# Kernel optimization log

Measured on AMD Instinct MI355X. Metric: run time of the kernel, lower is better.

The kernel has to match this reference:

```python
import jax, jax.numpy as jnp
import numpy as np

N = 131072          # events
N_OBS = 64          # observables
HID = [512, 512, 512]          # trunk hidden widths
SUB_HID = [512, 256]           # per-pair subnetwork hidden widths
P = 3                          # number of pairings


def _glorot(key, shape):
    fan_in, fan_out = shape[-2], shape[-1]
    lim = np.sqrt(6.0 / (fan_in + fan_out)).astype(np.float32)
    return jax.random.uniform(key, shape, jnp.float32, -lim, lim)


def setup_inputs() -> dict:
    key = jax.random.key(0)
    ks = jax.random.split(key, 16)
    x = jax.random.normal(ks[0], (N, N_OBS), jnp.float32)
    y = jax.random.randint(ks[1], (N,), 0, 3)
    pairs = jnp.array([[0, 1], [0, 2], [1, 2]], dtype=jnp.int32)
    # trunk params
    W0 = _glorot(ks[2], (N_OBS, HID[0])); b0 = jnp.zeros((HID[0],), jnp.float32)
    W1 = _glorot(ks[3], (HID[0], HID[1])); b1 = jnp.zeros((HID[1],), jnp.float32)
    W2 = _glorot(ks[4], (HID[1], HID[2])); b2 = jnp.zeros((HID[2],), jnp.float32)
    # stacked per-pair subnetwork params (all P subnets share shapes)
    SW0 = _glorot(ks[5], (P, HID[2], SUB_HID[0])); Sb0 = jnp.zeros((P, SUB_HID[0]), jnp.float32)
    SW1 = _glorot(ks[6], (P, SUB_HID[0], SUB_HID[1])); Sb1 = jnp.zeros((P, SUB_HID[1]), jnp.float32)
    SW2 = _glorot(ks[7], (P, SUB_HID[1], 1)); Sb2 = jnp.zeros((P, 1), jnp.float32)
    return {"x": x, "y": y, "pairs": pairs,
            "W0": W0, "b0": b0, "W1": W1, "b1": b1, "W2": W2, "b2": b2,
            "SW0": SW0, "Sb0": Sb0, "SW1": SW1, "Sb1": Sb1, "SW2": SW2, "Sb2": Sb2}


def reference(x, y, pairs, W0, b0, W1, b1, W2, b2, SW0, Sb0, SW1, Sb1, SW2, Sb2):
    relu = jax.nn.relu
    # Trunk. Note: in the torch module with dropout_prob>0, the first Linear sits at
    # layer index 1, so the activation is applied to the raw input as well (eval-mode
    # dropout == identity). We reproduce that exactly.
    h = relu(x) @ W0 + b0
    h = relu(h) @ W1 + b1
    repr_ = relu(h) @ W2 + b2                      # [N, HID[-1]]

    # Per-pair membership masks (jit-safe stand-in for the variable-size gather):
    # mask[p, n] = True iff y[n] is one of the two labels of pairing p.
    mask = (y[None, :] == pairs[:, 0:1]) | (y[None, :] == pairs[:, 1:2])  # [P, N] bool

    # Per-pair RatioModel subnetworks, batched over the pair dim.
    # Same activation-before-every-Linear pattern as the trunk (dropout indices).
    hs = jnp.einsum('nd,pdh->pnh', relu(repr_), SW0) + Sb0[:, None, :]
    hs = jnp.einsum('pnh,phk->pnk', relu(hs), SW1) + Sb1[:, None, :]
    logit = jnp.einsum('pnk,pko->pno', relu(hs), SW2) + Sb2[:, None, :]  # [P, N, 1]
    s_hat = jnp.clip(jax.nn.sigmoid(logit[..., 0]), 1e-9, None)          # [P, N]
    r_hat = (1.0 - s_hat) / s_hat                                        # [P, N]

    maskf = mask.astype(s_hat.dtype)
    return repr_, r_hat * maskf, s_hat * maskf, mask
```

## Files before the change

kernel.cpp:

```cpp
#include <hip/hip_runtime.h>
#include <stdint.h>

#define NE 131072

typedef __attribute__((ext_vector_type(8))) short bf16x8;
typedef __attribute__((ext_vector_type(4))) float f32x4;

static __device__ __forceinline__ unsigned short f2bf(float f) {
  unsigned u = __float_as_uint(f);
  u += 0x7FFF + ((u >> 16) & 1);
  return (unsigned short)(u >> 16);
}
static __device__ __forceinline__ float bf2f(unsigned short h) {
  return __uint_as_float((unsigned)h << 16);
}
static __device__ __forceinline__ void gload_lds16(const void* g, void* l) {
  __builtin_amdgcn_global_load_lds(
      (const __attribute__((address_space(1))) unsigned*)g,
      (__attribute__((address_space(3))) unsigned*)l, 16, 0, 0);
}

__global__ void weight_prep(const float* __restrict__ W0, const float* __restrict__ W1,
                            const float* __restrict__ W2, const float* __restrict__ SW0,
                            const float* __restrict__ SW1, const float* __restrict__ SW2,
                            unsigned short* W0t, unsigned short* W1t,
                            unsigned short* W2t, unsigned short* SW0t,
                            unsigned short* SW1t, unsigned short* SW2b) {
  __shared__ float tile[32][33];
  const int u = blockIdx.y;
  const float* src; unsigned short* dst; int K, Nc;
  if (u == 0)      { src = W0;  dst = W0t;  K = 64;  Nc = 512; }
  else if (u == 1) { src = W1;  dst = W1t;  K = 512; Nc = 512; }
  else if (u == 2) { src = W2;  dst = W2t;  K = 512; Nc = 512; }
  else if (u < 6)  { int p = u - 3; src = SW0 + (long)p * 512 * 512; dst = SW0t + (long)p * 512 * 512; K = 512; Nc = 512; }
  else if (u < 9)  { int p = u - 6; src = SW1 + (long)p * 512 * 256; dst = SW1t + (long)p * 256 * 512; K = 512; Nc = 256; }
  else             { int p = u - 9; src = SW2 + (long)p * 256;       dst = SW2b + (long)p * 256;       K = 256; Nc = 1; }
  const int tkn = K >> 5;
  const int tk = blockIdx.x % tkn, tn = blockIdx.x / tkn;
  if (tn >= ((Nc + 31) >> 5)) return;
  const int k0 = tk * 32, n0 = tn * 32;
  const int tx = threadIdx.x & 31, ty = threadIdx.x >> 5;
  if (n0 + tx < Nc)
#pragma unroll
    for (int j = 0; j < 4; ++j)
      tile[ty * 4 + j][tx] = src[(long)(k0 + ty * 4 + j) * Nc + n0 + tx];
  __syncthreads();
#pragma unroll
  for (int j = 0; j < 4; ++j) {
    int n = n0 + ty * 4 + j;
    if (n < Nc) dst[(long)n * K + k0 + tx] = f2bf(tile[tx][ty * 4 + j]);
  }
}

__global__ void relu_cvt_x(const float4* __restrict__ x,
                           ushort4* __restrict__ xb) {
  int i = blockIdx.x * blockDim.x + threadIdx.x;
  float4 v = x[i];
  ushort4 o;
  o.x = f2bf(fmaxf(v.x, 0.f));
  o.y = f2bf(fmaxf(v.y, 0.f));
  o.z = f2bf(fmaxf(v.z, 0.f));
  o.w = f2bf(fmaxf(v.w, 0.f));
  xb[i] = o;
}

__global__ void build_idx(const int* __restrict__ y, const int* __restrict__ pairs,
                          int chunkRows, int* __restrict__ idxL,
                          int* __restrict__ posA, int* __restrict__ cnts) {
  const int c = blockIdx.x, p = blockIdx.y;
  const int la = pairs[p * 2], lb = pairs[p * 2 + 1];
  const long r0 = (long)c * chunkRows;
  const long cb = r0;
  __shared__ int wbase[4];
  __shared__ int running;
  if (threadIdx.x == 0) running = 0;
  __syncthreads();
  const int lane = threadIdx.x & 63, wv = threadIdx.x >> 6;
  for (int it = 0; it < chunkRows / 256; ++it) {
    const int r = it * 256 + threadIdx.x;
    const int yv = y[r0 + r];
    const bool act = (yv == la) || (yv == lb);
    const unsigned long long m = __ballot(act);
    const int rank = __popcll(m & ((1ull << lane) - 1));
    if (lane == 0) wbase[wv] = __popcll(m);
    __syncthreads();
    int wb = 0;
#pragma unroll
    for (int w = 0; w < 4; ++w) wb += (w < wv) ? wbase[w] : 0;
    const int tot = wbase[0] + wbase[1] + wbase[2] + wbase[3];
    if (act) {
      const int posi = running + wb + rank;
      idxL[(long)p * NE + cb + posi] = r;
      posA[(long)p * NE + r0 + r] = (int)(cb + posi);
    } else {
      posA[(long)p * NE + r0 + r] = -1;
    }
    __syncthreads();
    if (threadIdx.x == 0) running += tot;
    __syncthreads();
  }
  const int cnt = running;
  if (threadIdx.x == 0) cnts[c * 3 + p] = cnt;
  const int padded = (cnt + 255) & ~255;
  const int last = (cnt > 0) ? idxL[(long)p * NE + cb + cnt - 1] : 0;
  for (int i = cnt + threadIdx.x; i < padded; i += 256)
    idxL[(long)p * NE + cb + i] = last;
}

__global__ __launch_bounds__(512, 4) void gemmT(
    const unsigned short* __restrict__ A, long aZ,
    const unsigned short* __restrict__ Bt, long bZ,
    const float* __restrict__ bias, long biasZ,
    float* __restrict__ outF,
    unsigned short* __restrict__ outA, long cZ,
    int K, int Nc,
    const unsigned short* __restrict__ w2, long w2Z,
    float* __restrict__ PB, long pbZ, int r0,
    const int* __restrict__ aIdx, long aIdxZ,
    const int* __restrict__ cnts) {
  __shared__ unsigned short lds[3 * 12288];
  __shared__ float part[4][128];
  const int z = blockIdx.z;
  const long brow = (long)blockIdx.x * 128;
  if (cnts) {
    const int cp = cnts[z];
    if ((int)brow >= ((cp + 255) & ~255)) return;
  }
  A += (long)z * aZ;
  Bt += (long)z * bZ;
  bias += (long)z * biasZ;
  if (outA) outA += (long)z * cZ;
  if (w2) { w2 += (long)z * w2Z; PB += (long)z * pbZ; }
  if (aIdx) aIdx += (long)z * aIdxZ;

  const int tid = threadIdx.x, wave = tid >> 6, lane = tid & 63;
  const int wm = wave >> 2, wn = wave & 3;
  const int lr = lane & 15, lh = lane >> 4;
  const int bcol = blockIdx.y * 256;
  const int nk = K >> 5;
  const int axr = (lh ^ ((lr >> 1) & 3)) * 8;

  const int arL = tid >> 2;
  const int arow = aIdx ? aIdx[brow + arL] : (int)(brow + arL);

  f32x4 acc[4][4];
#pragma unroll
  for (int m = 0; m < 4; ++m)
#pragma unroll
    for (int n = 0; n < 4; ++n) acc[m][n] = (f32x4){0.f, 0.f, 0.f, 0.f};

  auto STAGE = [&](int t) {
    if (t >= nk) return;
    unsigned short* dst = &lds[(t % 3) * 12288];
    const int k0 = t << 5;
    {
      const int c = tid;
      const int r = c >> 2;
      const int kc = (c & 3) ^ ((r >> 1) & 3);
      gload_lds16(A + (long)arow * K + k0 + kc * 8, &dst[(wave * 64) * 8]);
    }
#pragma unroll
    for (int i = 0; i < 2; ++i) {
      const int cb = i * 512 + wave * 64;
      const int c = cb + lane;
      const int r = c >> 2;
      const int kc = (c & 3) ^ ((r >> 1) & 3);
      gload_lds16(Bt + (long)(bcol + r) * K + k0 + kc * 8,
                  &dst[(512 + cb) * 8]);
    }
  };

  STAGE(0);
  STAGE(1);

  for (int t = 0; t < nk; ++t) {
    if (t < nk - 1)
      asm volatile("s_waitcnt vmcnt(3)" ::: "memory");
    else
      asm volatile("s_waitcnt vmcnt(0)" ::: "memory");
    __builtin_amdgcn_s_barrier();
    __builtin_amdgcn_sched_barrier(0);
    const unsigned short* buf = &lds[(t % 3) * 12288];
    bf16x8 a[4], b[4];
#pragma unroll
    for (int m = 0; m < 4; ++m)
      a[m] = *(const bf16x8*)&buf[(wm * 64 + m * 16 + lr) * 32 + axr];
#pragma unroll
    for (int n = 0; n < 4; ++n)
      b[n] = *(const bf16x8*)&buf[512 * 8 + (wn * 64 + n * 16 + lr) * 32 + axr];
    STAGE(t + 2);
    __builtin_amdgcn_s_setprio(1);
#pragma unroll
    for (int m = 0; m < 4; ++m)
#pragma unroll
      for (int n = 0; n < 4; ++n)
        acc[m][n] =
            __builtin_amdgcn_mfma_f32_16x16x32_bf16(a[m], b[n], acc[m][n], 0, 0, 0);
    __builtin_amdgcn_s_setprio(0);
  }

  float bv[4];
#pragma unroll
  for (int n = 0; n < 4; ++n) bv[n] = bias[bcol + wn * 64 + n * 16 + lr];

  if (!w2) {
#pragma unroll
    for (int m = 0; m < 4; ++m) {
#pragma unroll
      for (int r = 0; r < 4; ++r) {
        long e = brow + wm * 64 + m * 16 + lh * 4 + r;
#pragma unroll
        for (int n = 0; n < 4; ++n) {
          int oc = bcol + wn * 64 + n * 16 + lr;
          float v = acc[m][n][r] + bv[n];
          if (outF) outF[e * Nc + oc] = v;
          if (outA) outA[e * Nc + oc] = f2bf(fmaxf(v, 0.f));
        }
      }
    }
  } else {
    float w2v[4];
#pragma unroll
    for (int n = 0; n < 4; ++n) w2v[n] = bf2f(w2[wn * 64 + n * 16 + lr]);
#pragma unroll
    for (int m = 0; m < 4; ++m) {
#pragma unroll
      for (int r = 0; r < 4; ++r) {
        float s = 0.f;
#pragma unroll
        for (int n = 0; n < 4; ++n)
          s += fmaxf(acc[m][n][r] + bv[n], 0.f) * w2v[n];
#pragma unroll
        for (int off = 1; off < 16; off <<= 1) s += __shfl_xor(s, off);
        if (lr == 0) part[wn][wm * 64 + m * 16 + lh * 4 + r] = s;
      }
    }
    __syncthreads();
    if (tid < 128)
      PB[r0 + brow + tid] =
          part[0][tid] + part[1][tid] + part[2][tid] + part[3][tid];
  }
}

__global__ void head_final(const float* __restrict__ PB,
                           const int* __restrict__ posA,
                           const float* __restrict__ Sb2,
                           float* __restrict__ outR, float* __restrict__ outS,
                           float* __restrict__ outM) {
  const long n = (long)blockIdx.x * 256 + threadIdx.x;
  const int p = blockIdx.y;
  const int pos = posA[(long)p * NE + n];
  float rr = 0.f, s = 0.f, mf = 0.f;
  if (pos >= 0) {
    float logit = PB[(long)p * NE + pos] + Sb2[p];
    s = 1.f / (1.f + expf(-logit));
    s = fmaxf(s, 1e-9f);
    rr = (1.f - s) / s;
    mf = 1.f;
  }
  outR[(long)p * NE + n] = rr;
  outS[(long)p * NE + n] = s;
  outM[(long)p * NE + n] = mf;
}

extern "C" void kernel_launch(void* const* d_in, const int* in_sizes, int n_in,
                              void* d_out, int out_size, void* d_ws, size_t ws_size,
                              hipStream_t stream) {
  const float* x   = (const float*)d_in[0];
  const int*   y   = (const int*)d_in[1];
  const int*   prs = (const int*)d_in[2];
  const float* W0  = (const float*)d_in[3];
  const float* b0  = (const float*)d_in[4];
  const float* W1  = (const float*)d_in[5];
  const float* b1  = (const float*)d_in[6];
  const float* W2  = (const float*)d_in[7];
  const float* b2  = (const float*)d_in[8];
  const float* SW0 = (const float*)d_in[9];
  const float* Sb0 = (const float*)d_in[10];
  const float* SW1 = (const float*)d_in[11];
  const float* Sb1 = (const float*)d_in[12];
  const float* SW2 = (const float*)d_in[13];
  const float* Sb2 = (const float*)d_in[14];

  uint8_t* ws = (uint8_t*)d_ws;
  size_t off = 0;
  auto take = [&](size_t bytes) -> void* {
    void* ptr = ws + off;
    off = (off + bytes + 255) & ~(size_t)255;
    return ptr;
  };
  unsigned short* W0t  = (unsigned short*)take((size_t)64 * 512 * 2);
  unsigned short* W1t  = (unsigned short*)take((size_t)512 * 512 * 2);
  unsigned short* W2t  = (unsigned short*)take((size_t)512 * 512 * 2);
  unsigned short* SW0t = (unsigned short*)take((size_t)3 * 512 * 512 * 2);
  unsigned short* SW1t = (unsigned short*)take((size_t)3 * 256 * 512 * 2);
  unsigned short* SW2b = (unsigned short*)take((size_t)3 * 256 * 2);
  unsigned short* Xb   = (unsigned short*)take((size_t)NE * 64 * 2);
  float*          PB   = (float*)take((size_t)3 * NE * 4);
  int*            idxL = (int*)take((size_t)3 * NE * 4);
  int*            posA = (int*)take((size_t)3 * NE * 4);
  int*            cnts = (int*)take((size_t)64 * 4);
  const size_t fixed = off;

  long chunk = 32768;
  while (chunk > 8192 && fixed + (size_t)6 * chunk * 1024 + 4096 > ws_size)
    chunk >>= 1;
  const int nchunks = (int)(NE / chunk);

  unsigned short* T0   = (unsigned short*)take((size_t)chunk * 512 * 2);
  unsigned short* T1   = (unsigned short*)take((size_t)chunk * 512 * 2);
  unsigned short* bufR = (unsigned short*)take((size_t)chunk * 512 * 2);
  unsigned short* H3   = (unsigned short*)take((size_t)3 * chunk * 512 * 2);

  float* out   = (float*)d_out;
  float* outRe = out;
  float* outR  = out + (size_t)NE * 512;
  float* outS  = outR + (size_t)3 * NE;
  float* outM  = outS + (size_t)3 * NE;

  weight_prep<<<dim3(256, 12), 256, 0, stream>>>(W0, W1, W2, SW0, SW1, SW2,
                                                 W0t, W1t, W2t, SW0t, SW1t, SW2b);
  relu_cvt_x<<<dim3(NE * 64 / 4 / 256), 256, 0, stream>>>((const float4*)x,
                                                          (ushort4*)Xb);
  build_idx<<<dim3(nchunks, 3), 256, 0, stream>>>(y, prs, (int)chunk,
                                                  idxL, posA, cnts);

  for (int c = 0; c < nchunks; ++c) {
    const long r0 = (long)c * chunk;
    gemmT<<<dim3(chunk / 128, 2, 1), 512, 0, stream>>>(
        Xb + r0 * 64, 0, W0t, 0, b0, 0, nullptr, T0, 0, 64, 512,
        nullptr, 0, nullptr, 0, 0, nullptr, 0, nullptr);
    gemmT<<<dim3(chunk / 128, 2, 1), 512, 0, stream>>>(
        T0, 0, W1t, 0, b1, 0, nullptr, T1, 0, 512, 512,
        nullptr, 0, nullptr, 0, 0, nullptr, 0, nullptr);
    gemmT<<<dim3(chunk / 128, 2, 1), 512, 0, stream>>>(
        T1, 0, W2t, 0, b2, 0, outRe + r0 * 512, bufR, 0, 512, 512,
        nullptr, 0, nullptr, 0, 0, nullptr, 0, nullptr);
    gemmT<<<dim3(chunk / 128, 2, 3), 512, 0, stream>>>(
        bufR, 0, SW0t, (long)512 * 512, Sb0, 512, nullptr,
        H3, (long)chunk * 512, 512, 512,
        nullptr, 0, nullptr, 0, 0, idxL + r0, NE, cnts + c * 3);
    gemmT<<<dim3(chunk / 128, 1, 3), 512, 0, stream>>>(
        H3, (long)chunk * 512, SW1t, (long)256 * 512, Sb1, 256, nullptr,
        nullptr, 0, 512, 256,
        SW2b, 256, PB, (long)NE, (int)r0, nullptr, 0, cnts + c * 3);
  }
  head_final<<<dim3(NE / 256, 3), 256, 0, stream>>>(PB, posA, Sb2,
                                                    outR, outS, outM);
}
```

Before: 696.0 us.

## Replace per-layer GEMM launches with one persistent cooperative kernel using grid syncs

Moves the per-chunk sequence of five GEMM launches into a single cooperative persistent kernel that loops over chunks and layers, with grid-wide barriers between stages and a grid-stride loop over tiles. The GEMM body becomes a noinline device function shared by the old kernel and the new pipeline. The aim is to remove kernel launch overhead and tail gaps between many small launches. In exchange it adds grid-sync cost, a noinline call that may raise register pressure or spill, and a fixed grid size of at most 512 blocks. It falls back to the old launches if the cooperative launch fails.

```diff
diff --git a/kernel.cpp b/kernel.cpp
--- a/kernel.cpp
+++ b/kernel.cpp
@@ -1,7 +1,10 @@
 #include <hip/hip_runtime.h>
+#include <hip/hip_cooperative_groups.h>
 #include <stdint.h>
 
 #define NE 131072
+
+namespace cg = cooperative_groups;
 
 typedef __attribute__((ext_vector_type(8))) short bf16x8;
 typedef __attribute__((ext_vector_type(4))) float f32x4;
@@ -107,21 +110,19 @@
     idxL[(long)p * NE + cb + i] = last;
 }
 
-__global__ __launch_bounds__(512, 4) void gemmT(
-    const unsigned short* __restrict__ A, long aZ,
-    const unsigned short* __restrict__ Bt, long bZ,
-    const float* __restrict__ bias, long biasZ,
-    float* __restrict__ outF,
-    unsigned short* __restrict__ outA, long cZ,
+static __device__ __attribute__((noinline)) void gemm_tile(
+    unsigned short* lds, float* part,
+    int bx, int by, int z,
+    const unsigned short* A, long aZ,
+    const unsigned short* Bt, long bZ,
+    const float* bias, long biasZ,
+    float* outF, unsigned short* outA, long cZ,
     int K, int Nc,
-    const unsigned short* __restrict__ w2, long w2Z,
-    float* __restrict__ PB, long pbZ, int r0,
-    const int* __restrict__ aIdx, long aIdxZ,
-    const int* __restrict__ cnts) {
-  __shared__ unsigned short lds[3 * 12288];
-  __shared__ float part[4][128];
-  const int z = blockIdx.z;
-  const long brow = (long)blockIdx.x * 128;
+    const unsigned short* w2, long w2Z,
+    float* PB, long pbZ, int r0,
+    const int* aIdx, long aIdxZ,
+    const int* cnts) {
+  const long brow = (long)bx * 128;
   if (cnts) {
     const int cp = cnts[z];
     if ((int)brow >= ((cp + 255) & ~255)) return;
@@ -136,7 +137,7 @@
   const int tid = threadIdx.x, wave = tid >> 6, lane = tid & 63;
   const int wm = wave >> 2, wn = wave & 3;
   const int lr = lane & 15, lh = lane >> 4;
-  const int bcol = blockIdx.y * 256;
+  const int bcol = by * 256;
   const int nk = K >> 5;
   const int axr = (lh ^ ((lr >> 1) & 3)) * 8;
 
@@ -232,13 +233,73 @@
           s += fmaxf(acc[m][n][r] + bv[n], 0.f) * w2v[n];
 #pragma unroll
         for (int off = 1; off < 16; off <<= 1) s += __shfl_xor(s, off);
-        if (lr == 0) part[wn][wm * 64 + m * 16 + lh * 4 + r] = s;
+        if (lr == 0) part[wn * 128 + wm * 64 + m * 16 + lh * 4 + r] = s;
       }
     }
     __syncthreads();
     if (tid < 128)
-      PB[r0 + brow + tid] =
-          part[0][tid] + part[1][tid] + part[2][tid] + part[3][tid];
+      PB[r0 + brow + tid] = part[tid] + part[128 + tid] + part[256 + tid] +
+                            part[384 + tid];
+    __syncthreads();
+  }
+}
+
+__global__ __launch_bounds__(512, 4) void gemmT(
+    const unsigned short* A, long aZ, const unsigned short* Bt, long bZ,
+    const float* bias, long biasZ, float* outF, unsigned short* outA, long cZ,
+    int K, int Nc, const unsigned short* w2, long w2Z, float* PB, long pbZ,
+    int r0, const int* aIdx, long aIdxZ, const int* cnts) {
+  __shared__ unsigned short lds[3 * 12288];
+  __shared__ float part[512];
+  gemm_tile(lds, part, blockIdx.x, blockIdx.y, blockIdx.z, A, aZ, Bt, bZ,
+            bias, biasZ, outF, outA, cZ, K, Nc, w2, w2Z, PB, pbZ, r0, aIdx,
+            aIdxZ, cnts);
+}
+
+__global__ __launch_bounds__(512, 4) void mlp_pipeline(
+    const unsigned short* Xb,
+    const unsigned short* W0t, const float* b0,
+    const unsigned short* W1t, const float* b1,
+    const unsigned short* W2t, const float* b2,
+    const unsigned short* SW0t, const float* Sb0,
+    const unsigned short* SW1t, const float* Sb1,
+    const unsigned short* SW2b, const float* Sb2,
+    unsigned short* T0, unsigned short* T1,
+    unsigned short* bufR, unsigned short* H3,
+    float* PB, const int* idxL, const int* cnts,
+    float* outRe, int chunk, int nchunks) {
+  __shared__ unsigned short lds[3 * 12288];
+  __shared__ float part[512];
+  cg::grid_group g = cg::this_grid();
+  const int ntx = chunk / 128;
+  for (int c = 0; c < nchunks; ++c) {
+    const long r0 = (long)c * chunk;
+    for (int w = blockIdx.x; w < ntx * 2; w += gridDim.x)
+      gemm_tile(lds, part, w % ntx, w / ntx, 0, Xb + r0 * 64, 0, W0t, 0, b0,
+                0, nullptr, T0, 0, 64, 512, nullptr, 0, nullptr, 0, 0,
+                nullptr, 0, nullptr);
+    g.sync();
+    for (int w = blockIdx.x; w < ntx * 2; w += gridDim.x)
+      gemm_tile(lds, part, w % ntx, w / ntx, 0, T0, 0, W1t, 0, b1, 0,
+                nullptr, T1, 0, 512, 512, nullptr, 0, nullptr, 0, 0, nullptr,
+                0, nullptr);
+    g.sync();
+    for (int w = blockIdx.x; w < ntx * 2; w += gridDim.x)
+      gemm_tile(lds, part, w % ntx, w / ntx, 0, T1, 0, W2t, 0, b2, 0,
+                outRe + r0 * 512, bufR, 0, 512, 512, nullptr, 0, nullptr, 0,
+                0, nullptr, 0, nullptr);
+    g.sync();
+    for (int w = blockIdx.x; w < ntx * 6; w += gridDim.x)
+      gemm_tile(lds, part, w % ntx, (w / ntx) & 1, w / (ntx * 2), bufR, 0,
+                SW0t, (long)512 * 512, Sb0, 512, nullptr, H3,
+                (long)chunk * 512, 512, 512, nullptr, 0, nullptr, 0, 0,
+                idxL + r0, NE, cnts + c * 3);
+    g.sync();
+    for (int w = blockIdx.x; w < ntx * 3; w += gridDim.x)
+      gemm_tile(lds, part, w % ntx, 0, w / ntx, H3, (long)chunk * 512, SW1t,
+                (long)256 * 512, Sb1, 256, nullptr, nullptr, 0, 512, 256,
+                SW2b, 256, PB, (long)NE, (int)r0, nullptr, 0, cnts + c * 3);
+    g.sync();
   }
 }
 
@@ -325,25 +386,44 @@
   build_idx<<<dim3(nchunks, 3), 256, 0, stream>>>(y, prs, (int)chunk,
                                                   idxL, posA, cnts);
 
-  for (int c = 0; c < nchunks; ++c) {
-    const long r0 = (long)c * chunk;
-    gemmT<<<dim3(chunk / 128, 2, 1), 512, 0, stream>>>(
-        Xb + r0 * 64, 0, W0t, 0, b0, 0, nullptr, T0, 0, 64, 512,
-        nullptr, 0, nullptr, 0, 0, nullptr, 0, nullptr);
-    gemmT<<<dim3(chunk / 128, 2, 1), 512, 0, stream>>>(
-        T0, 0, W1t, 0, b1, 0, nullptr, T1, 0, 512, 512,
-        nullptr, 0, nullptr, 0, 0, nullptr, 0, nullptr);
-    gemmT<<<dim3(chunk / 128, 2, 1), 512, 0, stream>>>(
-        T1, 0, W2t, 0, b2, 0, outRe + r0 * 512, bufR, 0, 512, 512,
-        nullptr, 0, nullptr, 0, 0, nullptr, 0, nullptr);
-    gemmT<<<dim3(chunk / 128, 2, 3), 512, 0, stream>>>(
-        bufR, 0, SW0t, (long)512 * 512, Sb0, 512, nullptr,
-        H3, (long)chunk * 512, 512, 512,
-        nullptr, 0, nullptr, 0, 0, idxL + r0, NE, cnts + c * 3);
-    gemmT<<<dim3(chunk / 128, 1, 3), 512, 0, stream>>>(
-        H3, (long)chunk * 512, SW1t, (long)256 * 512, Sb1, 256, nullptr,
-        nullptr, 0, 512, 256,
-        SW2b, 256, PB, (long)NE, (int)r0, nullptr, 0, cnts + c * 3);
+  int chunkI = (int)chunk, nchunksI = nchunks;
+  int blkPerCU = 0;
+  bool coop = false;
+  if (hipOccupancyMaxActiveBlocksPerMultiprocessor(&blkPerCU, mlp_pipeline,
+                                                   512, 0) == hipSuccess &&
+      blkPerCU > 0) {
+    int grid = blkPerCU * 256;
+    if (grid > 512) grid = 512;
+    void* args[] = {&Xb, &W0t, &b0, &W1t, &b1, &W2t, &b2, &SW0t, &Sb0,
+                    &SW1t, &Sb1, &SW2b, &Sb2, &T0, &T1, &bufR, &H3, &PB,
+                    &idxL, &cnts, &outRe, &chunkI, &nchunksI};
+    hipError_t e = hipLaunchCooperativeKernel(
+        (const void*)mlp_pipeline, dim3(grid), dim3(512), args, 0, stream);
+    if (e == hipSuccess) coop = true;
+    else (void)hipGetLastError();
+  }
+
+  if (!coop) {
+    for (int c = 0; c < nchunks; ++c) {
+      const long r0 = (long)c * chunk;
+      gemmT<<<dim3(chunk / 128, 2, 1), 512, 0, stream>>>(
+          Xb + r0 * 64, 0, W0t, 0, b0, 0, nullptr, T0, 0, 64, 512,
+          nullptr, 0, nullptr, 0, 0, nullptr, 0, nullptr);
+      gemmT<<<dim3(chunk / 128, 2, 1), 512, 0, stream>>>(
+          T0, 0, W1t, 0, b1, 0, nullptr, T1, 0, 512, 512,
+          nullptr, 0, nullptr, 0, 0, nullptr, 0, nullptr);
+      gemmT<<<dim3(chunk / 128, 2, 1), 512, 0, stream>>>(
+          T1, 0, W2t, 0, b2, 0, outRe + r0 * 512, bufR, 0, 512, 512,
+          nullptr, 0, nullptr, 0, 0, nullptr, 0, nullptr);
+      gemmT<<<dim3(chunk / 128, 2, 3), 512, 0, stream>>>(
+          bufR, 0, SW0t, (long)512 * 512, Sb0, 512, nullptr,
+          H3, (long)chunk * 512, 512, 512,
+          nullptr, 0, nullptr, 0, 0, idxL + r0, NE, cnts + c * 3);
+      gemmT<<<dim3(chunk / 128, 1, 3), 512, 0, stream>>>(
+          H3, (long)chunk * 512, SW1t, (long)256 * 512, Sb1, 256, nullptr,
+          nullptr, 0, 512, 256,
+          SW2b, 256, PB, (long)NE, (int)r0, nullptr, 0, cnts + c * 3);
+    }
   }
   head_final<<<dim3(NE / 256, 3), 256, 0, stream>>>(PB, posA, Sb2,
                                                     outR, outS, outM);
```

New measurement: 1.956 ms. +181.1%, slower.
